# Kernel tuning notes

Measured on AMD Instinct MI355X. Metric: run time of the kernel, lower is better.

## Reference

```python
import jax, jax.numpy as jnp
import numpy as np

INPUT_DIM, ATTN_DIM, OUTPUT_DIM = 1024, 1024, 1024
B, LQ, LKV = 4, 2048, 2048


def setup_inputs() -> dict:
    key = jax.random.key(0)
    ks = jax.random.split(key, 10)
    s = 1.0 / np.sqrt(INPUT_DIM)
    return {
        "primary": jax.random.normal(ks[0], (B, LQ, INPUT_DIM), jnp.float32),
        "context_sequence": jax.random.normal(ks[1], (B, LKV, INPUT_DIM), jnp.float32),
        "mask": jax.random.randint(ks[2], (B, LQ, LKV), 0, 2).astype(jnp.float32),
        "Wq": jax.random.uniform(ks[3], (INPUT_DIM, ATTN_DIM), jnp.float32, -s, s),
        "bq": jax.random.uniform(ks[4], (ATTN_DIM,), jnp.float32, -s, s),
        "Wk": jax.random.uniform(ks[5], (INPUT_DIM, ATTN_DIM), jnp.float32, -s, s),
        "bk": jax.random.uniform(ks[6], (ATTN_DIM,), jnp.float32, -s, s),
        "Wv": jax.random.uniform(ks[7], (INPUT_DIM, OUTPUT_DIM), jnp.float32, -s, s),
        "bv": jax.random.uniform(ks[8], (OUTPUT_DIM,), jnp.float32, -s, s),
    }


def reference(primary, context_sequence, mask, Wq, bq, Wk, bk, Wv, bv):
    q = primary @ Wq + bq                      # [B, Lq, attn_dim]
    k = context_sequence @ Wk + bk             # [B, Lkv, attn_dim]
    v = context_sequence @ Wv + bv             # [B, Lkv, output_dim]
    score = jnp.einsum('bqd,bkd->bqk', q, k) / jnp.sqrt(jnp.float32(ATTN_DIM))
    score = score + mask * (-1e9)
    attn = jax.nn.softmax(score, axis=-1)
    return jnp.einsum('bqk,bkd->bqd', attn, v)  # [B, Lq, output_dim]
```

## Files before the change

kernel.cpp:

```cpp
#include <hip/hip_runtime.h>
#include <stdint.h>

typedef unsigned short u16;
typedef __bf16 bf16_t;
typedef bf16_t bf16x8 __attribute__((ext_vector_type(8)));
typedef float f32x4 __attribute__((ext_vector_type(4)));
typedef u16 u16x4 __attribute__((ext_vector_type(4)));
typedef u16 u16x8 __attribute__((ext_vector_type(8)));

__device__ __forceinline__ u16 f2bf(float f) {
  union { float f; uint32_t u; } v;
  v.f = f;
  uint32_t u = v.u + 0x7fffu + ((v.u >> 16) & 1u);
  return (u16)(u >> 16);
}

__device__ __forceinline__ float bf2f(u16 x) {
  union { uint32_t u; float f; } v;
  v.u = ((uint32_t)x) << 16;
  return v.f;
}

__device__ __forceinline__ void gload16(const void* g, void* l) {
  __builtin_amdgcn_global_load_lds(
      (__attribute__((address_space(1))) void*)g,
      (__attribute__((address_space(3))) void*)l, 16, 0, 0);
}

__device__ __forceinline__ f32x4 mfma16(bf16x8 a, bf16x8 b, f32x4 c) {
  return __builtin_amdgcn_mfma_f32_16x16x32_bf16(a, b, c, 0, 0, 0);
}

__global__ void cvt_f32_bf16(const float* __restrict__ in, u16* __restrict__ out, int n4) {
  int i = blockIdx.x * blockDim.x + threadIdx.x;
  int stride = gridDim.x * blockDim.x;
  for (; i < n4; i += stride) {
    float4 v = *((const float4*)in + i);
    u16x4 o;
    o.x = f2bf(v.x); o.y = f2bf(v.y); o.z = f2bf(v.z); o.w = f2bf(v.w);
    *((u16x4*)out + i) = o;
  }
}

__global__ void wt_transpose(const float* __restrict__ Wq, const float* __restrict__ Wk,
                             const float* __restrict__ Wv, u16* __restrict__ Oq,
                             u16* __restrict__ Ok, u16* __restrict__ Ov) {
  const float* W = blockIdx.z == 0 ? Wq : (blockIdx.z == 1 ? Wk : Wv);
  u16* O = blockIdx.z == 0 ? Oq : (blockIdx.z == 1 ? Ok : Ov);
  __shared__ float t[32][33];
  int x = threadIdx.x, y = threadIdx.y;
  int n0 = blockIdx.x * 32, k0 = blockIdx.y * 32;
#pragma unroll
  for (int i = 0; i < 32; i += 8)
    t[y + i][x] = W[(size_t)(k0 + y + i) * 1024 + n0 + x];
  __syncthreads();
#pragma unroll
  for (int i = 0; i < 32; i += 8)
    O[(size_t)(n0 + y + i) * 1024 + k0 + x] = f2bf(t[x][y + i]);
}

template <typename CT>
__global__ __launch_bounds__(512, 2) void gemm256(
    const u16* __restrict__ A, const u16* __restrict__ Bt,
    const float* __restrict__ bc0, const float* __restrict__ bc1,
    const float* __restrict__ biasRow,
    CT* __restrict__ C, int K, int lda, int ldb, int ldc,
    long long bsA, long long bsB, long long bsC) {
  A += (size_t)blockIdx.z * bsA;
  Bt += (size_t)blockIdx.z * bsB;
  C += (size_t)blockIdx.z * bsC;
  const float* biasCol = (blockIdx.z == 1) ? bc1 : bc0;

  __shared__ u16 lds[2][2][256 * 64];
  int tid = threadIdx.x;
  int lane = tid & 63, w = tid >> 6;
  int l15 = lane & 15, g = lane >> 4;
  int wr = w >> 2, wc = w & 3;
  int bm = blockIdx.x * 256, bn = blockIdx.y * 256;
  int NT = K >> 6;

  f32x4 acc[8][4] = {};

  auto stageA = [&](int buf, int h, int tk) {
    int k0 = tk * 64;
    int r = tid >> 3, cd = (tid & 7) * 8;
    int cs = cd ^ ((r & 7) * 8);
    int row0 = h * 64 + r;
    gload16(A + (size_t)(bm + row0) * lda + k0 + cs, &lds[buf][0][row0 * 64 + cd]);
    int row1 = row0 + 128;
    gload16(A + (size_t)(bm + row1) * lda + k0 + cs, &lds[buf][0][row1 * 64 + cd]);
  };
  auto stageB = [&](int buf, int x, int tk) {
    int k0 = tk * 64;
#pragma unroll
    for (int l = 0; l < 2; ++l) {
      int u = l * 512 + tid;
      int r = u >> 3, cd = (u & 7) * 8;
      int cs = cd ^ ((r & 7) * 8);
      int row = x * 128 + r;
      gload16(Bt + (size_t)(bn + row) * ldb + k0 + cs, &lds[buf][1][row * 64 + cd]);
    }
  };
  auto ldA = [&](int buf, int m, int kc) -> bf16x8 {
    int row = wr * 128 + m * 16 + l15;
    int col = (kc * 32 + g * 8) ^ ((row & 7) * 8);
    return *(const bf16x8*)&lds[buf][0][row * 64 + col];
  };
  auto ldB = [&](int buf, int j, int kc) -> bf16x8 {
    int row = wc * 64 + j * 16 + l15;
    int col = (kc * 32 + g * 8) ^ ((row & 7) * 8);
    return *(const bf16x8*)&lds[buf][1][row * 64 + col];
  };

  stageA(0, 0, 0);
  stageB(0, 0, 0);
  stageB(0, 1, 0);
  stageA(0, 1, 0);
  int t1c = NT > 1 ? 1 : 0;
  stageA(1, 0, t1c);
  stageB(1, 0, t1c);
  asm volatile("s_waitcnt vmcnt(6)" ::: "memory");
  __builtin_amdgcn_s_barrier();

  for (int t = 0; t < NT; ++t) {
    int cur = t & 1, nxt = cur ^ 1;
    int tn1 = (t + 1 < NT) ? t + 1 : NT - 1;
    int tn2 = (t + 2 < NT) ? t + 2 : NT - 1;
    bf16x8 a0[4], b0[4], b1[4];

#pragma unroll
    for (int i = 0; i < 4; ++i) a0[i] = ldA(cur, i, 0);
#pragma unroll
    for (int j = 0; j < 4; ++j) b0[j] = ldB(cur, j, 0);
    stageB(nxt, 1, tn1);
    __builtin_amdgcn_s_barrier();
    asm volatile("s_waitcnt lgkmcnt(0)" ::: "memory");
    __builtin_amdgcn_sched_barrier(0);
    __builtin_amdgcn_s_setprio(1);
#pragma unroll
    for (int i = 0; i < 4; ++i)
#pragma unroll
      for (int j = 0; j < 4; ++j) acc[i][j] = mfma16(a0[i], b0[j], acc[i][j]);
    __builtin_amdgcn_s_setprio(0);
    __builtin_amdgcn_s_barrier();

#pragma unroll
    for (int i = 0; i < 4; ++i) a0[i] = ldA(cur, i, 1);
#pragma unroll
    for (int j = 0; j < 4; ++j) b1[j] = ldB(cur, j, 1);
    stageA(nxt, 1, tn1);
    __builtin_amdgcn_s_barrier();
    asm volatile("s_waitcnt lgkmcnt(0)" ::: "memory");
    __builtin_amdgcn_sched_barrier(0);
    __builtin_amdgcn_s_setprio(1);
#pragma unroll
    for (int i = 0; i < 4; ++i)
#pragma unroll
      for (int j = 0; j < 4; ++j) acc[i][j] = mfma16(a0[i], b1[j], acc[i][j]);
    __builtin_amdgcn_s_setprio(0);
    asm volatile("s_waitcnt vmcnt(8)" ::: "memory");
    __builtin_amdgcn_s_barrier();

#pragma unroll
    for (int i = 0; i < 4; ++i) a0[i] = ldA(cur, 4 + i, 0);
    stageA(cur, 0, tn2);
    __builtin_amdgcn_s_barrier();
    asm volatile("s_waitcnt lgkmcnt(0)" ::: "memory");
    __builtin_amdgcn_sched_barrier(0);
    __builtin_amdgcn_s_setprio(1);
#pragma unroll
    for (int i = 0; i < 4; ++i)
#pragma unroll
      for (int j = 0; j < 4; ++j) acc[4 + i][j] = mfma16(a0[i], b0[j], acc[4 + i][j]);
    __builtin_amdgcn_s_setprio(0);
    __builtin_amdgcn_s_barrier();

#pragma unroll
    for (int i = 0; i < 4; ++i) a0[i] = ldA(cur, 4 + i, 1);
    stageB(cur, 0, tn2);
    __builtin_amdgcn_s_barrier();
    asm volatile("s_waitcnt lgkmcnt(0)" ::: "memory");
    __builtin_amdgcn_sched_barrier(0);
    __builtin_amdgcn_s_setprio(1);
#pragma unroll
    for (int i = 0; i < 4; ++i)
#pragma unroll
      for (int j = 0; j < 4; ++j) acc[4 + i][j] = mfma16(a0[i], b1[j], acc[4 + i][j]);
    __builtin_amdgcn_s_setprio(0);
    asm volatile("s_waitcnt vmcnt(6)" ::: "memory");
    __builtin_amdgcn_s_barrier();
  }

#pragma unroll
  for (int mi = 0; mi < 8; ++mi) {
    int row = bm + wr * 128 + mi * 16 + g * 4;
#pragma unroll
    for (int j = 0; j < 4; ++j) {
      int col = bn + wc * 64 + j * 16 + l15;
      float bcv = biasCol ? biasCol[col] : 0.0f;
#pragma unroll
      for (int rr = 0; rr < 4; ++rr) {
        float brv = biasRow ? biasRow[row + rr] : 0.0f;
        float v = acc[mi][j][rr] + bcv + brv;
        if constexpr (sizeof(CT) == 2)
          C[(size_t)(row + rr) * ldc + col] = f2bf(v);
        else
          C[(size_t)(row + rr) * ldc + col] = v;
      }
    }
  }
}

__global__ __launch_bounds__(256) void softmax_mask(
    const u16* __restrict__ S, const float* __restrict__ mask, u16* __restrict__ P) {
  const float C1 = 0.04508422f;
  const float C2 = -1.4426950e9f;
  int wid = (blockIdx.x * blockDim.x + threadIdx.x) >> 6;
  int lane = threadIdx.x & 63;
  size_t base = (size_t)wid * 2048;
  const u16* sp = S + base;
  const float* mp = mask + base;

  float a[32];
#pragma unroll
  for (int pass = 0; pass < 4; ++pass) {
    int e0 = pass * 512 + lane * 8;
    u16x8 sv = *(const u16x8*)(sp + e0);
    float4 m0 = *(const float4*)(mp + e0);
    float4 m1 = *(const float4*)(mp + e0 + 4);
    a[pass * 8 + 0] = bf2f(sv[0]) * C1 + m0.x * C2;
    a[pass * 8 + 1] = bf2f(sv[1]) * C1 + m0.y * C2;
    a[pass * 8 + 2] = bf2f(sv[2]) * C1 + m0.z * C2;
    a[pass * 8 + 3] = bf2f(sv[3]) * C1 + m0.w * C2;
    a[pass * 8 + 4] = bf2f(sv[4]) * C1 + m1.x * C2;
    a[pass * 8 + 5] = bf2f(sv[5]) * C1 + m1.y * C2;
    a[pass * 8 + 6] = bf2f(sv[6]) * C1 + m1.z * C2;
    a[pass * 8 + 7] = bf2f(sv[7]) * C1 + m1.w * C2;
  }
  float m = a[0];
#pragma unroll
  for (int i = 1; i < 32; ++i) m = fmaxf(m, a[i]);
#pragma unroll
  for (int off = 32; off >= 1; off >>= 1) m = fmaxf(m, __shfl_xor(m, off));

  float s = 0.0f;
#pragma unroll
  for (int i = 0; i < 32; ++i) {
    a[i] = exp2f(a[i] - m);
    s += a[i];
  }
#pragma unroll
  for (int off = 32; off >= 1; off >>= 1) s += __shfl_xor(s, off);
  float inv = 1.0f / s;

  u16* pp = P + base;
#pragma unroll
  for (int pass = 0; pass < 4; ++pass) {
    int e0 = pass * 512 + lane * 8;
    u16x8 o;
#pragma unroll
    for (int j = 0; j < 8; ++j) o[j] = f2bf(a[pass * 8 + j] * inv);
    *(u16x8*)(pp + e0) = o;
  }
}

extern "C" void kernel_launch(void* const* d_in, const int* in_sizes, int n_in,
                              void* d_out, int out_size, void* d_ws, size_t ws_size,
                              hipStream_t stream) {
  const float* primary = (const float*)d_in[0];
  const float* ctx     = (const float*)d_in[1];
  const float* mask    = (const float*)d_in[2];
  const float* Wq      = (const float*)d_in[3];
  const float* bq      = (const float*)d_in[4];
  const float* Wk      = (const float*)d_in[5];
  const float* bk      = (const float*)d_in[6];
  const float* Wv      = (const float*)d_in[7];
  const float* bv      = (const float*)d_in[8];
  float* out = (float*)d_out;

  char* ws = (char*)d_ws;
  u16* qbf     = (u16*)(ws);
  u16* kbf     = (u16*)(ws + 16777216);
  u16* vtbf    = (u16*)(ws + 2 * 16777216);
  u16* prim_bf = (u16*)(ws + 3 * 16777216);
  u16* ctx_bf  = (u16*)(ws + 4 * 16777216);
  u16* wqt     = (u16*)(ws + 5 * 16777216);
  u16* wkt     = (u16*)(ws + 5 * 16777216 + 2097152);
  u16* wvt     = (u16*)(ws + 5 * 16777216 + 2 * 2097152);
  u16* sbf     = (u16*)(ws + 3 * 16777216);
  u16* pbf     = (u16*)(ws);

  cvt_f32_bf16<<<2048, 256, 0, stream>>>(primary, prim_bf, 8388608 / 4);
  cvt_f32_bf16<<<2048, 256, 0, stream>>>(ctx, ctx_bf, 8388608 / 4);
  wt_transpose<<<dim3(32, 32, 3), dim3(32, 8), 0, stream>>>(Wq, Wk, Wv, wqt, wkt, wvt);

  gemm256<u16><<<dim3(32, 4, 2), 512, 0, stream>>>(
      prim_bf, wqt, bq, bk, nullptr, qbf, 1024, 1024, 1024, 1024,
      8192 * 1024LL, 1024 * 1024LL, 8192 * 1024LL);
  gemm256<u16><<<dim3(4, 32, 1), 512, 0, stream>>>(
      wvt, ctx_bf, nullptr, nullptr, bv, vtbf, 1024, 1024, 1024, 8192, 0, 0, 0);
  gemm256<u16><<<dim3(8, 8, 4), 512, 0, stream>>>(
      qbf, kbf, nullptr, nullptr, nullptr, sbf, 1024, 1024, 1024, 2048,
      2048 * 1024LL, 2048 * 1024LL, 2048 * 2048LL);
  softmax_mask<<<2048, 256, 0, stream>>>(sbf, mask, pbf);
  gemm256<float><<<dim3(8, 4, 4), 512, 0, stream>>>(
      pbf, vtbf, nullptr, nullptr, nullptr, out, 2048, 2048, 8192, 1024,
      2048 * 2048LL, 2048LL, 2048 * 1024LL);
}
```

Baseline: 240.6 us.

## Double-buffer LDS fragment reads in GEMM and remap blocks across XCDs

The GEMM main loop now loads the next A/B register fragments from LDS while the current MFMA batch runs, using two register sets and partial lgkmcnt waits in place of full waits before each compute phase. Block indices are also remapped so consecutive linear blocks are spread across the eight XCD groups, meant to improve L2 locality for tiles that share operands. This adds register pressure and changes the order of barriers and waits, so a wrong wait count could cause races.

Result: no change. 243.5 us (+1.2%).

```diff
diff --git a/kernel.cpp b/kernel.cpp
--- a/kernel.cpp
+++ b/kernel.cpp
@@ -66,17 +66,23 @@
     const float* __restrict__ biasRow,
     CT* __restrict__ C, int K, int lda, int ldb, int ldc,
     long long bsA, long long bsB, long long bsC) {
-  A += (size_t)blockIdx.z * bsA;
-  Bt += (size_t)blockIdx.z * bsB;
-  C += (size_t)blockIdx.z * bsC;
-  const float* biasCol = (blockIdx.z == 1) ? bc1 : bc0;
+  int nx = gridDim.x, ny = gridDim.y;
+  int lin = blockIdx.x + nx * (blockIdx.y + ny * blockIdx.z);
+  int q = (nx * ny * gridDim.z) >> 3;
+  int s = (lin & 7) * q + (lin >> 3);
+  int bx = s % nx, by = (s / nx) % ny, bz = s / (nx * ny);
+
+  A += (size_t)bz * bsA;
+  Bt += (size_t)bz * bsB;
+  C += (size_t)bz * bsC;
+  const float* biasCol = (bz == 1) ? bc1 : bc0;
 
   __shared__ u16 lds[2][2][256 * 64];
   int tid = threadIdx.x;
   int lane = tid & 63, w = tid >> 6;
   int l15 = lane & 15, g = lane >> 4;
   int wr = w >> 2, wc = w & 3;
-  int bm = blockIdx.x * 256, bn = blockIdx.y * 256;
+  int bm = bx * 256, bn = by * 256;
   int NT = K >> 6;
 
   f32x4 acc[8][4] = {};
@@ -126,13 +132,58 @@
     int cur = t & 1, nxt = cur ^ 1;
     int tn1 = (t + 1 < NT) ? t + 1 : NT - 1;
     int tn2 = (t + 2 < NT) ? t + 2 : NT - 1;
-    bf16x8 a0[4], b0[4], b1[4];
-
-#pragma unroll
-    for (int i = 0; i < 4; ++i) a0[i] = ldA(cur, i, 0);
+    bf16x8 ac[4], ad[4], b0[4], b1[4];
+
+#pragma unroll
+    for (int i = 0; i < 4; ++i) ac[i] = ldA(cur, i, 0);
 #pragma unroll
     for (int j = 0; j < 4; ++j) b0[j] = ldB(cur, j, 0);
     stageB(nxt, 1, tn1);
+    __builtin_amdgcn_s_barrier();
+#pragma unroll
+    for (int i = 0; i < 4; ++i) ad[i] = ldA(cur, i, 1);
+#pragma unroll
+    for (int j = 0; j < 4; ++j) b1[j] = ldB(cur, j, 1);
+    asm volatile("s_waitcnt lgkmcnt(8)" ::: "memory");
+    __builtin_amdgcn_sched_barrier(0);
+    __builtin_amdgcn_s_setprio(1);
+#pragma unroll
+    for (int i = 0; i < 4; ++i)
+#pragma unroll
+      for (int j = 0; j < 4; ++j) acc[i][j] = mfma16(ac[i], b0[j], acc[i][j]);
+    __builtin_amdgcn_s_setprio(0);
+    asm volatile("s_waitcnt vmcnt(6)" ::: "memory");
+    __builtin_amdgcn_s_barrier();
+
+    stageA(nxt, 1, tn1);
+    __builtin_amdgcn_s_barrier();
+#pragma unroll
+    for (int i = 0; i < 4; ++i) ac[i] = ldA(cur, 4 + i, 0);
+    asm volatile("s_waitcnt lgkmcnt(4)" ::: "memory");
+    __builtin_amdgcn_sched_barrier(0);
+    __builtin_amdgcn_s_setprio(1);
+#pragma unroll
+    for (int i = 0; i < 4; ++i)
+#pragma unroll
+      for (int j = 0; j < 4; ++j) acc[i][j] = mfma16(ad[i], b1[j], acc[i][j]);
+    __builtin_amdgcn_s_setprio(0);
+    __builtin_amdgcn_s_barrier();
+
+    stageA(cur, 0, tn2);
+    __builtin_amdgcn_s_barrier();
+#pragma unroll
+    for (int i = 0; i < 4; ++i) ad[i] = ldA(cur, 4 + i, 1);
+    asm volatile("s_waitcnt lgkmcnt(4)" ::: "memory");
+    __builtin_amdgcn_sched_barrier(0);
+    __builtin_amdgcn_s_setprio(1);
+#pragma unroll
+    for (int i = 0; i < 4; ++i)
+#pragma unroll
+      for (int j = 0; j < 4; ++j) acc[4 + i][j] = mfma16(ac[i], b0[j], acc[4 + i][j]);
+    __builtin_amdgcn_s_setprio(0);
+    __builtin_amdgcn_s_barrier();
+
+    stageB(cur, 0, tn2);
     __builtin_amdgcn_s_barrier();
     asm volatile("s_waitcnt lgkmcnt(0)" ::: "memory");
     __builtin_amdgcn_sched_barrier(0);
@@ -140,52 +191,7 @@
 #pragma unroll
     for (int i = 0; i < 4; ++i)
 #pragma unroll
-      for (int j = 0; j < 4; ++j) acc[i][j] = mfma16(a0[i], b0[j], acc[i][j]);
-    __builtin_amdgcn_s_setprio(0);
-    __builtin_amdgcn_s_barrier();
-
-#pragma unroll
-    for (int i = 0; i < 4; ++i) a0[i] = ldA(cur, i, 1);
-#pragma unroll
-    for (int j = 0; j < 4; ++j) b1[j] = ldB(cur, j, 1);
-    stageA(nxt, 1, tn1);
-    __builtin_amdgcn_s_barrier();
-    asm volatile("s_waitcnt lgkmcnt(0)" ::: "memory");
-    __builtin_amdgcn_sched_barrier(0);
-    __builtin_amdgcn_s_setprio(1);
-#pragma unroll
-    for (int i = 0; i < 4; ++i)
-#pragma unroll
-      for (int j = 0; j < 4; ++j) acc[i][j] = mfma16(a0[i], b1[j], acc[i][j]);
-    __builtin_amdgcn_s_setprio(0);
-    asm volatile("s_waitcnt vmcnt(8)" ::: "memory");
-    __builtin_amdgcn_s_barrier();
-
-#pragma unroll
-    for (int i = 0; i < 4; ++i) a0[i] = ldA(cur, 4 + i, 0);
-    stageA(cur, 0, tn2);
-    __builtin_amdgcn_s_barrier();
-    asm volatile("s_waitcnt lgkmcnt(0)" ::: "memory");
-    __builtin_amdgcn_sched_barrier(0);
-    __builtin_amdgcn_s_setprio(1);
-#pragma unroll
-    for (int i = 0; i < 4; ++i)
-#pragma unroll
-      for (int j = 0; j < 4; ++j) acc[4 + i][j] = mfma16(a0[i], b0[j], acc[4 + i][j]);
-    __builtin_amdgcn_s_setprio(0);
-    __builtin_amdgcn_s_barrier();
-
-#pragma unroll
-    for (int i = 0; i < 4; ++i) a0[i] = ldA(cur, 4 + i, 1);
-    stageB(cur, 0, tn2);
-    __builtin_amdgcn_s_barrier();
-    asm volatile("s_waitcnt lgkmcnt(0)" ::: "memory");
-    __builtin_amdgcn_sched_barrier(0);
-    __builtin_amdgcn_s_setprio(1);
-#pragma unroll
-    for (int i = 0; i < 4; ++i)
-#pragma unroll
-      for (int j = 0; j < 4; ++j) acc[4 + i][j] = mfma16(a0[i], b1[j], acc[4 + i][j]);
+      for (int j = 0; j < 4; ++j) acc[4 + i][j] = mfma16(ad[i], b1[j], acc[4 + i][j]);
     __builtin_amdgcn_s_setprio(0);
     asm volatile("s_waitcnt vmcnt(6)" ::: "memory");
     __builtin_amdgcn_s_barrier();
```

## Reschedule global-to-LDS staging in 256x256 GEMM main loop

Applied to the files above, without the earlier changes.

Splits the shared LDS array into separate A and B buffers and reorders when each half-tile of A and B is prefetched within the four-phase loop. The full B tile for the tile after next is now issued together in the third phase, the next A half goes out in the first phase, and the vmcnt waits change to match. Separate register arrays for the two k-chunks of A let their fragment loads overlap with MFMAs. The aim is to spread global-load issue more evenly and cut stalls, at the cost of more registers and a riskier wait-count and buffer-reuse ordering.

New measurement: 268.8 us. 11.7% more time.

```diff
diff --git a/kernel.cpp b/kernel.cpp
--- a/kernel.cpp
+++ b/kernel.cpp
@@ -71,7 +71,8 @@
   C += (size_t)blockIdx.z * bsC;
   const float* biasCol = (blockIdx.z == 1) ? bc1 : bc0;
 
-  __shared__ u16 lds[2][2][256 * 64];
+  __shared__ u16 aLds[2][256 * 64];
+  __shared__ u16 bLds[2][256 * 64];
   int tid = threadIdx.x;
   int lane = tid & 63, w = tid >> 6;
   int l15 = lane & 15, g = lane >> 4;
@@ -86,9 +87,9 @@
     int r = tid >> 3, cd = (tid & 7) * 8;
     int cs = cd ^ ((r & 7) * 8);
     int row0 = h * 64 + r;
-    gload16(A + (size_t)(bm + row0) * lda + k0 + cs, &lds[buf][0][row0 * 64 + cd]);
+    gload16(A + (size_t)(bm + row0) * lda + k0 + cs, &aLds[buf][row0 * 64 + cd]);
     int row1 = row0 + 128;
-    gload16(A + (size_t)(bm + row1) * lda + k0 + cs, &lds[buf][0][row1 * 64 + cd]);
+    gload16(A + (size_t)(bm + row1) * lda + k0 + cs, &aLds[buf][row1 * 64 + cd]);
   };
   auto stageB = [&](int buf, int x, int tk) {
     int k0 = tk * 64;
@@ -98,18 +99,18 @@
       int r = u >> 3, cd = (u & 7) * 8;
       int cs = cd ^ ((r & 7) * 8);
       int row = x * 128 + r;
-      gload16(Bt + (size_t)(bn + row) * ldb + k0 + cs, &lds[buf][1][row * 64 + cd]);
+      gload16(Bt + (size_t)(bn + row) * ldb + k0 + cs, &bLds[buf][row * 64 + cd]);
     }
   };
   auto ldA = [&](int buf, int m, int kc) -> bf16x8 {
     int row = wr * 128 + m * 16 + l15;
     int col = (kc * 32 + g * 8) ^ ((row & 7) * 8);
-    return *(const bf16x8*)&lds[buf][0][row * 64 + col];
+    return *(const bf16x8*)&aLds[buf][row * 64 + col];
   };
   auto ldB = [&](int buf, int j, int kc) -> bf16x8 {
     int row = wc * 64 + j * 16 + l15;
     int col = (kc * 32 + g * 8) ^ ((row & 7) * 8);
-    return *(const bf16x8*)&lds[buf][1][row * 64 + col];
+    return *(const bf16x8*)&bLds[buf][row * 64 + col];
   };
 
   stageA(0, 0, 0);
@@ -119,20 +120,21 @@
   int t1c = NT > 1 ? 1 : 0;
   stageA(1, 0, t1c);
   stageB(1, 0, t1c);
-  asm volatile("s_waitcnt vmcnt(6)" ::: "memory");
+  stageB(1, 1, t1c);
+  asm volatile("s_waitcnt vmcnt(8)" ::: "memory");
   __builtin_amdgcn_s_barrier();
 
   for (int t = 0; t < NT; ++t) {
     int cur = t & 1, nxt = cur ^ 1;
     int tn1 = (t + 1 < NT) ? t + 1 : NT - 1;
     int tn2 = (t + 2 < NT) ? t + 2 : NT - 1;
-    bf16x8 a0[4], b0[4], b1[4];
-
-#pragma unroll
-    for (int i = 0; i < 4; ++i) a0[i] = ldA(cur, i, 0);
+    bf16x8 ac[4], ad[4], b0[4], b1[4];
+
+#pragma unroll
+    for (int i = 0; i < 4; ++i) ac[i] = ldA(cur, i, 0);
 #pragma unroll
     for (int j = 0; j < 4; ++j) b0[j] = ldB(cur, j, 0);
-    stageB(nxt, 1, tn1);
+    stageA(nxt, 1, tn1);
     __builtin_amdgcn_s_barrier();
     asm volatile("s_waitcnt lgkmcnt(0)" ::: "memory");
     __builtin_amdgcn_sched_barrier(0);
@@ -140,15 +142,14 @@
 #pragma unroll
     for (int i = 0; i < 4; ++i)
 #pragma unroll
-      for (int j = 0; j < 4; ++j) acc[i][j] = mfma16(a0[i], b0[j], acc[i][j]);
+      for (int j = 0; j < 4; ++j) acc[i][j] = mfma16(ac[i], b0[j], acc[i][j]);
     __builtin_amdgcn_s_setprio(0);
     __builtin_amdgcn_s_barrier();
 
 #pragma unroll
-    for (int i = 0; i < 4; ++i) a0[i] = ldA(cur, i, 1);
+    for (int i = 0; i < 4; ++i) ad[i] = ldA(cur, i, 1);
 #pragma unroll
     for (int j = 0; j < 4; ++j) b1[j] = ldB(cur, j, 1);
-    stageA(nxt, 1, tn1);
     __builtin_amdgcn_s_barrier();
     asm volatile("s_waitcnt lgkmcnt(0)" ::: "memory");
     __builtin_amdgcn_sched_barrier(0);
@@ -156,14 +157,16 @@
 #pragma unroll
     for (int i = 0; i < 4; ++i)
 #pragma unroll
-      for (int j = 0; j < 4; ++j) acc[i][j] = mfma16(a0[i], b1[j], acc[i][j]);
+      for (int j = 0; j < 4; ++j) acc[i][j] = mfma16(ad[i], b1[j], acc[i][j]);
     __builtin_amdgcn_s_setprio(0);
     asm volatile("s_waitcnt vmcnt(8)" ::: "memory");
     __builtin_amdgcn_s_barrier();
 
 #pragma unroll
-    for (int i = 0; i < 4; ++i) a0[i] = ldA(cur, 4 + i, 0);
+    for (int i = 0; i < 4; ++i) ac[i] = ldA(cur, 4 + i, 0);
     stageA(cur, 0, tn2);
+    stageB(cur, 0, tn2);
+    stageB(cur, 1, tn2);
     __builtin_amdgcn_s_barrier();
     asm volatile("s_waitcnt lgkmcnt(0)" ::: "memory");
     __builtin_amdgcn_sched_barrier(0);
@@ -171,13 +174,12 @@
 #pragma unroll
     for (int i = 0; i < 4; ++i)
 #pragma unroll
-      for (int j = 0; j < 4; ++j) acc[4 + i][j] = mfma16(a0[i], b0[j], acc[4 + i][j]);
+      for (int j = 0; j < 4; ++j) acc[4 + i][j] = mfma16(ac[i], b0[j], acc[4 + i][j]);
     __builtin_amdgcn_s_setprio(0);
     __builtin_amdgcn_s_barrier();
 
 #pragma unroll
-    for (int i = 0; i < 4; ++i) a0[i] = ldA(cur, 4 + i, 1);
-    stageB(cur, 0, tn2);
+    for (int i = 0; i < 4; ++i) ad[i] = ldA(cur, 4 + i, 1);
     __builtin_amdgcn_s_barrier();
     asm volatile("s_waitcnt lgkmcnt(0)" ::: "memory");
     __builtin_amdgcn_sched_barrier(0);
@@ -185,9 +187,9 @@
 #pragma unroll
     for (int i = 0; i < 4; ++i)
 #pragma unroll
-      for (int j = 0; j < 4; ++j) acc[4 + i][j] = mfma16(a0[i], b1[j], acc[4 + i][j]);
+      for (int j = 0; j < 4; ++j) acc[4 + i][j] = mfma16(ad[i], b1[j], acc[4 + i][j]);
     __builtin_amdgcn_s_setprio(0);
-    asm volatile("s_waitcnt vmcnt(6)" ::: "memory");
+    asm volatile("s_waitcnt vmcnt(8)" ::: "memory");
     __builtin_amdgcn_s_barrier();
   }
 
```
